# Kernel optimization log

Measured on AMD Instinct MI355X. Metric: run time of the kernel, lower is better.

The kernel has to match this reference:

```python
import jax, jax.numpy as jnp
import numpy as np

SIGMA = 1.0

def setup_inputs() -> dict:
    key = jax.random.key(0)
    k1, k2, k3 = jax.random.split(key, 3)
    X_new = jax.random.normal(k1, (8192, 128), dtype=jnp.float32)
    X_train = jax.random.normal(k2, (32768, 128), dtype=jnp.float32)
    atomic_weights = jax.random.normal(k3, (32768, 1), dtype=jnp.float32)
    return {"X_new": X_new, "X_train": X_train, "atomic_weights": atomic_weights}

def reference(X_new, X_train, atomic_weights):
    x2 = jnp.sum(X_new * X_new, axis=-1, keepdims=True)            # [N_new, 1]
    y2 = jnp.sum(X_train * X_train, axis=-1)                       # [N_train]
    cross = jnp.einsum('nd,md->nm', X_new, X_train)                # [N_new, N_train]
    dist_sq = jnp.maximum(x2 + y2[None, :] - 2.0 * cross, 0.0)
    K_new = jnp.exp(-dist_sq / (2.0 * SIGMA ** 2))
    per_atom_energy = K_new @ atomic_weights                       # [N_new, 1]
    return per_atom_energy
```

## Files before the change

### kernel.cpp

```cpp
#include <hip/hip_runtime.h>
#include <stdint.h>

typedef __attribute__((ext_vector_type(4))) int i32x4;
typedef __attribute__((ext_vector_type(16))) int i32x16;
typedef __attribute__((ext_vector_type(8))) short short8;
typedef __attribute__((ext_vector_type(16))) float f32x16;

#define LOG2E 1.4426950408889634f
#define S1 16.0f
#define S1_INV 0.0625f
#define S2 4096.0f
#define K2 (1.0f / 65536.0f)

__device__ inline float fast_exp2(float x) {
#if __has_builtin(__builtin_amdgcn_exp2f)
  return __builtin_amdgcn_exp2f(x);
#else
  float r;
  asm volatile("v_exp_f32 %0, %1" : "=v"(r) : "v"(x));
  return r;
#endif
}

__device__ inline void gload16(const void* g, void* l) {
  __builtin_amdgcn_global_load_lds(
      (const __attribute__((address_space(1))) void*)g,
      (__attribute__((address_space(3))) void*)l, 16, 0, 0);
}
__device__ inline void gload4(const void* g, void* l) {
  __builtin_amdgcn_global_load_lds(
      (const __attribute__((address_space(1))) void*)g,
      (__attribute__((address_space(3))) void*)l, 4, 0, 0);
}

__device__ inline void q4(float4 v, float pre, int& hw, int& lw) {
  float xs[4] = {v.x, v.y, v.z, v.w};
  int h = 0, l = 0;
#pragma unroll
  for (int j = 0; j < 4; ++j) {
    float x = xs[j] * pre;
    float hf = rintf(fminf(fmaxf(x * S1, -127.f), 127.f));
    float rf = x - hf * S1_INV;
    float lf = rintf(fminf(fmaxf(rf * S2, -127.f), 127.f));
    h |= ((int)hf & 255) << (8 * j);
    l |= ((int)lf & 255) << (8 * j);
  }
  hw = h;
  lw = l;
}

__global__ __launch_bounds__(256) void gk_conv_s(const float* __restrict__ Xtr,
                                                 const float* __restrict__ wts,
                                                 char* __restrict__ planes,
                                                 float* __restrict__ s, int M) {
  int g = blockIdx.x * 256 + threadIdx.x;
  int row = g >> 3;
  int gr = g & 7;
  if (row >= M) return;
  const float* p = Xtr + (size_t)row * 128 + gr * 16;
  int hw[4], lw[4];
  float ss = 0.f;
#pragma unroll
  for (int i = 0; i < 4; ++i) {
    float4 v = *(const float4*)(p + i * 4);
    ss += v.x * v.x + v.y * v.y + v.z * v.z + v.w * v.w;
    q4(v, 1.0f, hw[i], lw[i]);
  }
  ss += __shfl_xor(ss, 1, 64);
  ss += __shfl_xor(ss, 2, 64);
  ss += __shfl_xor(ss, 4, 64);
  if (gr == 0) s[row] = expf(-0.5f * ss) * wts[row];

  int T = row >> 5, r = row & 31;
  size_t base = (size_t)T * 8192 + (gr >> 1) * 1024 + (gr & 1) * 512 + r * 16;
  *(i32x4*)(planes + base) = (i32x4){hw[0], hw[1], hw[2], hw[3]};
  *(i32x4*)(planes + base + 4096) = (i32x4){lw[0], lw[1], lw[2], lw[3]};
}

__global__ __launch_bounds__(512, 4) void gk_main_i8(
    const float* __restrict__ Xnew, const char* __restrict__ planes,
    const float* __restrict__ s, float* __restrict__ out, int N, int M,
    int mchunk) {
  extern __shared__ char dlds[];

  const int t = threadIdx.x;
  const int l = t & 63;
  const int w = t >> 6;
  const int cl = l & 31;
  const int lk = l >> 5;

  const int n0 = blockIdx.x * 256;
  const int M0 = blockIdx.y * mchunk;
  const int iters = mchunk >> 5;
  const int T0 = M0 >> 5;

#define STAGE(tt)                                                       \
  {                                                                     \
    int st_ = ((tt) < iters) ? (tt) : (iters - 1);   \
    gload16(planes + (size_t)(T0 + st_) * 8192 + t * 16,                \
            dlds + ((tt)&3) * 8192 + t * 16);                           \
    gload4(s + M0 + st_ * 32 + l, dlds + 32768 + ((tt)&3) * 256);       \
  }

#define COMPUTE(acc_hh, acc_m, tile)                                    \
  {                                                                     \
    const char* buf_ = dlds + ((tile)&3) * 8192;                        \
    acc_hh = zero16;                                                    \
    acc_m = zero16;                                                     \
    __builtin_amdgcn_s_setprio(1);                                      \
    _Pragma("unroll") for (int kf = 0; kf < 4; ++kf) {                  \
      const char* kb_ = buf_ + kf * 1024 + lk * 512 + cl * 16;          \
      i32x4 ah_ = *(const i32x4*)(kb_);                                 \
      i32x4 al_ = *(const i32x4*)(kb_ + 4096);                          \
      acc_hh = __builtin_amdgcn_mfma_i32_32x32x32_i8(ah_, bh[kf], acc_hh, 0, 0, 0); \
      acc_m = __builtin_amdgcn_mfma_i32_32x32x32_i8(ah_, bl[kf], acc_m, 0, 0, 0);   \
      acc_m = __builtin_amdgcn_mfma_i32_32x32x32_i8(al_, bh[kf], acc_m, 0, 0, 0);   \
    }                                                                   \
    __builtin_amdgcn_s_setprio(0);                                      \
  }

#define EPI(acc_hh, acc_m, tile)                                        \
  {                                                                     \
    const float4* sl4_ =                                                \
        (const float4*)(dlds + 32768 + ((tile)&3) * 256);               \
    _Pragma("unroll") for (int q = 0; q < 4; ++q) {                     \
      float4 sv_ = sl4_[q * 2 + lk];                                    \
      _Pragma("unroll") for (int j = 0; j < 4; ++j) {                   \
        int r_ = q * 4 + j;                                             \
        float c_ = (float)((acc_hh[r_] << 8) + acc_m[r_]) * K2;         \
        out0 += fast_exp2(c_) * (&sv_.x)[j];                            \
      }                                                                 \
    }                                                                   \
  }

  const i32x16 zero16 = {0, 0, 0, 0, 0, 0, 0, 0, 0, 0, 0, 0, 0, 0, 0, 0};

  STAGE(0);
  STAGE(1);

  i32x4 bh[4], bl[4];
  float pref;
  {
    float ss = 0.f;
    const float* pc = Xnew + (size_t)(n0 + w * 32 + cl) * 128;
#pragma unroll
    for (int kf = 0; kf < 4; ++kf) {
      const float* p = pc + kf * 32 + lk * 16;
      int hw[4], lw[4];
#pragma unroll
      for (int i = 0; i < 4; ++i) {
        float4 v = *(const float4*)(p + i * 4);
        ss += v.x * v.x + v.y * v.y + v.z * v.z + v.w * v.w;
        q4(v, LOG2E, hw[i], lw[i]);
      }
      bh[kf] = (i32x4){hw[0], hw[1], hw[2], hw[3]};
      bl[kf] = (i32x4){lw[0], lw[1], lw[2], lw[3]};
    }
    ss += __shfl_xor(ss, 32, 64);
    pref = expf(-0.5f * ss);
  }

  float out0 = 0.f;
  i32x16 hhA, mA, hhB, mB;

  asm volatile("s_waitcnt vmcnt(2)" ::: "memory");
  __builtin_amdgcn_s_barrier();

  __builtin_amdgcn_sched_barrier(0);
  STAGE(2);
  COMPUTE(hhA, mA, 0);
  asm volatile("s_waitcnt vmcnt(2)" ::: "memory");
  __builtin_amdgcn_s_barrier();

#pragma unroll 1
  for (int tt = 1; tt < iters - 1; tt += 2) {
    __builtin_amdgcn_sched_barrier(0);
    STAGE(tt + 2);
    COMPUTE(hhB, mB, tt);
    EPI(hhA, mA, tt - 1);
    asm volatile("s_waitcnt vmcnt(2)" ::: "memory");
    __builtin_amdgcn_s_barrier();

    __builtin_amdgcn_sched_barrier(0);
    STAGE(tt + 3);
    COMPUTE(hhA, mA, tt + 1);
    EPI(hhB, mB, tt);
    asm volatile("s_waitcnt vmcnt(2)" ::: "memory");
    __builtin_amdgcn_s_barrier();
  }

  __builtin_amdgcn_sched_barrier(0);
  COMPUTE(hhB, mB, iters - 1);
  EPI(hhA, mA, iters - 2);
  EPI(hhB, mB, iters - 1);

  out0 += __shfl_xor(out0, 32, 64);
  if (l < 32) {
    int n = n0 + w * 32 + l;
    atomicAdd(out + n, pref * out0);
  }
#undef STAGE
#undef COMPUTE
#undef EPI
}

__global__ __launch_bounds__(256) void gk_prep(
    const float* __restrict__ Xnew, const float* __restrict__ Xtr,
    const float* __restrict__ w, float* __restrict__ s,
    float* __restrict__ pref, int M, int N) {
  int row = blockIdx.x * 4 + (threadIdx.x >> 6);
  int lane = threadIdx.x & 63;
  if (row >= M + N) return;
  const float* src =
      (row < M) ? (Xtr + (size_t)row * 128) : (Xnew + (size_t)(row - M) * 128);
  float2 v = *(const float2*)(src + lane * 2);
  float ss = v.x * v.x + v.y * v.y;
#pragma unroll
  for (int o = 32; o >= 1; o >>= 1) ss += __shfl_xor(ss, o, 64);
  if (lane == 0) {
    float e = expf(-0.5f * ss);
    if (row < M)
      s[row] = e * w[row];
    else
      pref[row - M] = e;
  }
}

__device__ inline unsigned swz_fb(unsigned off) {
  return off ^ (((off >> 8) & 7u) << 4);
}
__device__ inline void split8(float x0, float x1, float x2, float x3,
                              float x4, float x5, float x6, float x7,
                              float scale, short8& hi, short8& lo) {
  float xs[8] = {x0, x1, x2, x3, x4, x5, x6, x7};
#pragma unroll
  for (int i = 0; i < 8; ++i) {
    float v = xs[i] * scale;
    unsigned u = __float_as_uint(v);
    float hf = __uint_as_float(u & 0xffff0000u);
    float rr = v - hf;
    hi[i] = (short)(u >> 16);
    lo[i] = (short)(__float_as_uint(rr) >> 16);
  }
}

__global__ __launch_bounds__(256, 2) void gk_main_fb(
    const float* __restrict__ Xnew, const float* __restrict__ Xtr,
    const float* __restrict__ s, const float* __restrict__ pref,
    float* __restrict__ out, int N, int M, int mchunk) {
  __shared__ __attribute__((aligned(16))) char lds[33024];
  const int t = threadIdx.x;
  const int l = t & 63;
  const int w = t >> 6;
  const int lrow = l & 31;
  const int lk = l >> 5;
  const int n0 = blockIdx.x * 256;
  const int M0 = blockIdx.y * mchunk;
  const int iters = mchunk >> 6;

  short8 bh[2][8], bl[2][8];
  {
    const int colbase = n0 + w * 64;
#pragma unroll
    for (int nf = 0; nf < 2; ++nf) {
      int col = colbase + nf * 32 + lrow;
      const float* p = Xnew + (size_t)col * 128 + lk * 8;
#pragma unroll
      for (int kf = 0; kf < 8; ++kf) {
        float4 f0 = *(const float4*)(p + kf * 16);
        float4 f1 = *(const float4*)(p + kf * 16 + 4);
        split8(f0.x, f0.y, f0.z, f0.w, f1.x, f1.y, f1.z, f1.w, LOG2E,
               bh[nf][kf], bl[nf][kf]);
      }
    }
  }

  float out0 = 0.f, out1 = 0.f;
  float4 ga[4][2];
  float sreg = 0.f;
  {
    const float* abase = Xtr + (size_t)M0 * 128;
#pragma unroll
    for (int j = 0; j < 4; ++j) {
      int c = t + j * 256;
      int row = c >> 4, oct = c & 15;
      const float* p = abase + (size_t)row * 128 + oct * 8;
      ga[j][0] = *(const float4*)p;
      ga[j][1] = *(const float4*)(p + 4);
    }
    if (t < 64) sreg = s[M0 + t];
  }

#pragma unroll 1
  for (int it = 0; it < iters; ++it) {
    __syncthreads();
#pragma unroll
    for (int j = 0; j < 4; ++j) {
      int c = t + j * 256;
      int row = c >> 4, oct = c & 15;
      unsigned off = swz_fb((unsigned)(row * 256 + oct * 16));
      short8 hi, lo;
      split8(ga[j][0].x, ga[j][0].y, ga[j][0].z, ga[j][0].w, ga[j][1].x,
             ga[j][1].y, ga[j][1].z, ga[j][1].w, 1.0f, hi, lo);
      *(short8*)(lds + off) = hi;
      *(short8*)(lds + 16384 + off) = lo;
    }
    if (t < 64) *(float*)(lds + 32768 + t * 4) = sreg;
    __syncthreads();
    if (it + 1 < iters) {
      const float* abase = Xtr + (size_t)(M0 + (it + 1) * 64) * 128;
#pragma unroll
      for (int j = 0; j < 4; ++j) {
        int c = t + j * 256;
        int row = c >> 4, oct = c & 15;
        const float* p = abase + (size_t)row * 128 + oct * 8;
        ga[j][0] = *(const float4*)p;
        ga[j][1] = *(const float4*)(p + 4);
      }
      if (t < 64) sreg = s[M0 + (it + 1) * 64 + t];
    }
#pragma unroll
    for (int mf = 0; mf < 2; ++mf) {
      f32x16 acc0 = {0, 0, 0, 0, 0, 0, 0, 0, 0, 0, 0, 0, 0, 0, 0, 0};
      f32x16 acc1 = {0, 0, 0, 0, 0, 0, 0, 0, 0, 0, 0, 0, 0, 0, 0, 0};
#pragma unroll
      for (int kf = 0; kf < 8; ++kf) {
        unsigned off =
            swz_fb((unsigned)((mf * 32 + lrow) * 256 + kf * 32 + lk * 16));
        short8 ah = *(const short8*)(lds + off);
        short8 al = *(const short8*)(lds + 16384 + off);
        acc0 = __builtin_amdgcn_mfma_f32_32x32x16_bf16(ah, bh[0][kf], acc0, 0, 0, 0);
        acc1 = __builtin_amdgcn_mfma_f32_32x32x16_bf16(ah, bh[1][kf], acc1, 0, 0, 0);
        acc0 = __builtin_amdgcn_mfma_f32_32x32x16_bf16(ah, bl[0][kf], acc0, 0, 0, 0);
        acc1 = __builtin_amdgcn_mfma_f32_32x32x16_bf16(ah, bl[1][kf], acc1, 0, 0, 0);
        acc0 = __builtin_amdgcn_mfma_f32_32x32x16_bf16(al, bh[0][kf], acc0, 0, 0, 0);
        acc1 = __builtin_amdgcn_mfma_f32_32x32x16_bf16(al, bh[1][kf], acc1, 0, 0, 0);
      }
      const float* sl = (const float*)(lds + 32768 + mf * 128);
#pragma unroll
      for (int r = 0; r < 16; ++r) {
        int row = (r & 3) + 8 * (r >> 2) + 4 * lk;
        float sv = sl[row];
        out0 += fast_exp2(acc0[r]) * sv;
        out1 += fast_exp2(acc1[r]) * sv;
      }
    }
  }
  out0 += __shfl_xor(out0, 32, 64);
  out1 += __shfl_xor(out1, 32, 64);
  if (l < 32) {
    int n = n0 + w * 64 + l;
    atomicAdd(out + n, pref[n] * out0);
    n += 32;
    atomicAdd(out + n, pref[n] * out1);
  }
}

extern "C" void kernel_launch(void* const* d_in, const int* in_sizes, int n_in,
                              void* d_out, int out_size, void* d_ws,
                              size_t ws_size, hipStream_t stream) {
  const float* Xnew = (const float*)d_in[0];
  const float* Xtr = (const float*)d_in[1];
  const float* wts = (const float*)d_in[2];
  float* out = (float*)d_out;

  const int N = in_sizes[0] / 128;
  const int M = in_sizes[1] / 128;

  char* ws = (char*)d_ws;
  float* s_ws = (float*)ws;
  char* planes_ws = ws + (size_t)M * 4;
  const size_t need = (size_t)M * 4 + (size_t)M * 256;

  hipMemsetAsync(d_out, 0, (size_t)N * sizeof(float), stream);

  if (ws_size >= need) {
    gk_conv_s<<<dim3(M * 8 / 256), 256, 0, stream>>>(Xtr, wts, planes_ws,
                                                     s_ws, M);
    const int SPLIT = 16;
    dim3 grid(N / 256, SPLIT);
    gk_main_i8<<<grid, 512, 33792, stream>>>(Xnew, planes_ws, s_ws, out, N, M,
                                             M / SPLIT);
  } else {
    float* pref_ws = s_ws + M;
    int rows = M + N;
    gk_prep<<<dim3((rows + 3) / 4), 256, 0, stream>>>(Xnew, Xtr, wts, s_ws,
                                                      pref_ws, M, N);
    const int SPLIT = 16;
    dim3 grid(N / 256, SPLIT);
    gk_main_fb<<<grid, 256, 0, stream>>>(Xnew, Xtr, s_ws, pref_ws, out, N, M,
                                         M / SPLIT);
  }
}
```

Before: 122.4 us.

## Halve block size and interleave MFMAs with previous tile's exp epilogue

Blocks shrink from 512 to 256 threads (128 rows each), and each thread now issues two 16-byte global-to-LDS loads per stage so the 8 KB tile is still filled. The separate compute and epilogue phases are merged: each k-step's MFMAs are interleaved with the exp/accumulate work of the previous tile. Accumulators are zeroed after use, and setprio is dropped. The aim is to overlap MFMA latency with VALU exp work and raise occupancy via smaller blocks, at the cost of more LDS traffic per row and changed waitcnt accounting.

```diff
diff --git a/kernel.cpp b/kernel.cpp
--- a/kernel.cpp
+++ b/kernel.cpp
@@ -17,7 +17,7 @@
   return __builtin_amdgcn_exp2f(x);
 #else
   float r;
-  asm volatile("v_exp_f32 %0, %1" : "=v"(r) : "v"(x));
+  asm("v_exp_f32 %0, %1" : "=v"(r) : "v"(x));
   return r;
 #endif
 }
@@ -77,7 +77,7 @@
   *(i32x4*)(planes + base + 4096) = (i32x4){lw[0], lw[1], lw[2], lw[3]};
 }
 
-__global__ __launch_bounds__(512, 4) void gk_main_i8(
+__global__ __launch_bounds__(256, 4) void gk_main_i8(
     const float* __restrict__ Xnew, const char* __restrict__ planes,
     const float* __restrict__ s, float* __restrict__ out, int N, int M,
     int mchunk) {
@@ -89,25 +89,26 @@
   const int cl = l & 31;
   const int lk = l >> 5;
 
-  const int n0 = blockIdx.x * 256;
+  const int n0 = blockIdx.x * 128;
   const int M0 = blockIdx.y * mchunk;
   const int iters = mchunk >> 5;
   const int T0 = M0 >> 5;
 
+#define ZERO16 ((i32x16){0, 0, 0, 0, 0, 0, 0, 0, 0, 0, 0, 0, 0, 0, 0, 0})
+
 #define STAGE(tt)                                                       \
   {                                                                     \
     int st_ = ((tt) < iters) ? (tt) : (iters - 1);   \
-    gload16(planes + (size_t)(T0 + st_) * 8192 + t * 16,                \
-            dlds + ((tt)&3) * 8192 + t * 16);                           \
+    const char* src_ = planes + (size_t)(T0 + st_) * 8192 + t * 16;     \
+    char* dst_ = dlds + ((tt)&3) * 8192 + t * 16;                       \
+    gload16(src_, dst_);                                                \
+    gload16(src_ + 4096, dst_ + 4096);                                  \
     gload4(s + M0 + st_ * 32 + l, dlds + 32768 + ((tt)&3) * 256);       \
   }
 
-#define COMPUTE(acc_hh, acc_m, tile)                                    \
+#define MFMAS(acc_hh, acc_m, tile)                                      \
   {                                                                     \
     const char* buf_ = dlds + ((tile)&3) * 8192;                        \
-    acc_hh = zero16;                                                    \
-    acc_m = zero16;                                                     \
-    __builtin_amdgcn_s_setprio(1);                                      \
     _Pragma("unroll") for (int kf = 0; kf < 4; ++kf) {                  \
       const char* kb_ = buf_ + kf * 1024 + lk * 512 + cl * 16;          \
       i32x4 ah_ = *(const i32x4*)(kb_);                                 \
@@ -116,10 +117,9 @@
       acc_m = __builtin_amdgcn_mfma_i32_32x32x32_i8(ah_, bl[kf], acc_m, 0, 0, 0);   \
       acc_m = __builtin_amdgcn_mfma_i32_32x32x32_i8(al_, bh[kf], acc_m, 0, 0, 0);   \
     }                                                                   \
-    __builtin_amdgcn_s_setprio(0);                                      \
-  }
-
-#define EPI(acc_hh, acc_m, tile)                                        \
+  }
+
+#define EPI_RAW(acc_hh, acc_m, tile)                                    \
   {                                                                     \
     const float4* sl4_ =                                                \
         (const float4*)(dlds + 32768 + ((tile)&3) * 256);               \
@@ -133,7 +133,32 @@
     }                                                                   \
   }
 
-  const i32x16 zero16 = {0, 0, 0, 0, 0, 0, 0, 0, 0, 0, 0, 0, 0, 0, 0, 0};
+#define FUSED(accC_hh, accC_m, tileC, accP_hh, accP_m, tileP)           \
+  {                                                                     \
+    const char* buf_ = dlds + ((tileC)&3) * 8192;                       \
+    const float4* sl4_ =                                                \
+        (const float4*)(dlds + 32768 + ((tileP)&3) * 256);              \
+    _Pragma("unroll") for (int kf = 0; kf < 4; ++kf) {                  \
+      const char* kb_ = buf_ + kf * 1024 + lk * 512 + cl * 16;          \
+      i32x4 ah_ = *(const i32x4*)(kb_);                                 \
+      i32x4 al_ = *(const i32x4*)(kb_ + 4096);                          \
+      accC_hh = __builtin_amdgcn_mfma_i32_32x32x32_i8(ah_, bh[kf], accC_hh, 0, 0, 0); \
+      accC_m = __builtin_amdgcn_mfma_i32_32x32x32_i8(ah_, bl[kf], accC_m, 0, 0, 0);   \
+      accC_m = __builtin_amdgcn_mfma_i32_32x32x32_i8(al_, bh[kf], accC_m, 0, 0, 0);   \
+      float4 sv_ = sl4_[kf * 2 + lk];                                   \
+      _Pragma("unroll") for (int j = 0; j < 4; ++j) {                   \
+        int r_ = kf * 4 + j;                                            \
+        float c_ = (float)((accP_hh[r_] << 8) + accP_m[r_]) * K2;       \
+        out0 += fast_exp2(c_) * (&sv_.x)[j];                            \
+      }                                                                 \
+    }                                                                   \
+    accP_hh = ZERO16;                                                   \
+    accP_m = ZERO16;                                                    \
+  }
+
+#define REGION_END                                                      \
+  asm volatile("s_waitcnt vmcnt(3)" ::: "memory");                      \
+  __builtin_amdgcn_s_barrier();
 
   STAGE(0);
   STAGE(1);
@@ -161,38 +186,32 @@
   }
 
   float out0 = 0.f;
-  i32x16 hhA, mA, hhB, mB;
-
-  asm volatile("s_waitcnt vmcnt(2)" ::: "memory");
+  i32x16 hhA = ZERO16, mA = ZERO16, hhB = ZERO16, mB = ZERO16;
+
+  asm volatile("s_waitcnt vmcnt(3)" ::: "memory");
   __builtin_amdgcn_s_barrier();
 
   __builtin_amdgcn_sched_barrier(0);
   STAGE(2);
-  COMPUTE(hhA, mA, 0);
-  asm volatile("s_waitcnt vmcnt(2)" ::: "memory");
-  __builtin_amdgcn_s_barrier();
+  MFMAS(hhA, mA, 0);
+  REGION_END;
 
 #pragma unroll 1
   for (int tt = 1; tt < iters - 1; tt += 2) {
     __builtin_amdgcn_sched_barrier(0);
     STAGE(tt + 2);
-    COMPUTE(hhB, mB, tt);
-    EPI(hhA, mA, tt - 1);
-    asm volatile("s_waitcnt vmcnt(2)" ::: "memory");
-    __builtin_amdgcn_s_barrier();
+    FUSED(hhB, mB, tt, hhA, mA, tt - 1);
+    REGION_END;
 
     __builtin_amdgcn_sched_barrier(0);
     STAGE(tt + 3);
-    COMPUTE(hhA, mA, tt + 1);
-    EPI(hhB, mB, tt);
-    asm volatile("s_waitcnt vmcnt(2)" ::: "memory");
-    __builtin_amdgcn_s_barrier();
+    FUSED(hhA, mA, tt + 1, hhB, mB, tt);
+    REGION_END;
   }
 
   __builtin_amdgcn_sched_barrier(0);
-  COMPUTE(hhB, mB, iters - 1);
-  EPI(hhA, mA, iters - 2);
-  EPI(hhB, mB, iters - 1);
+  FUSED(hhB, mB, iters - 1, hhA, mA, iters - 2);
+  EPI_RAW(hhB, mB, iters - 1);
 
   out0 += __shfl_xor(out0, 32, 64);
   if (l < 32) {
@@ -200,8 +219,11 @@
     atomicAdd(out + n, pref * out0);
   }
 #undef STAGE
-#undef COMPUTE
-#undef EPI
+#undef MFMAS
+#undef EPI_RAW
+#undef FUSED
+#undef REGION_END
+#undef ZERO16
 }
 
 __global__ __launch_bounds__(256) void gk_prep(
@@ -378,8 +400,8 @@
     gk_conv_s<<<dim3(M * 8 / 256), 256, 0, stream>>>(Xtr, wts, planes_ws,
                                                      s_ws, M);
     const int SPLIT = 16;
-    dim3 grid(N / 256, SPLIT);
-    gk_main_i8<<<grid, 512, 33792, stream>>>(Xnew, planes_ws, s_ws, out, N, M,
+    dim3 grid(N / 128, SPLIT);
+    gk_main_i8<<<grid, 256, 33792, stream>>>(Xnew, planes_ws, s_ws, out, N, M,
                                              M / SPLIT);
   } else {
     float* pref_ws = s_ws + M;
```

Result: slower. 127.8 us (+4.4%).
